# Kernel tuning notes

Hardware: AMD Instinct MI355X
Metric: run time of the kernel (lower is better)

Reference implementation:

```python
import jax, jax.numpy as jnp
import numpy as np

B, N, K, D = 2, 32768, 16, 64
EPS = 1e-6

def setup_inputs() -> dict:
    key = jax.random.key(0)
    k1, k2, k3, k4, k5, k6 = jax.random.split(key, 6)
    coords = jax.random.normal(k1, (B, N, 3), dtype=jnp.float32)
    features = jax.random.normal(k2, (B, D, N, 1), dtype=jnp.float32)
    idx = jax.random.randint(k3, (B, N, K), 0, N, dtype=jnp.int32)
    dist = jax.random.uniform(k4, (B, N, K), dtype=jnp.float32)
    conv_w = jax.random.normal(k5, (D, 10), dtype=jnp.float32) * 0.3  # 1x1 conv weight
    conv_b = jax.random.normal(k6, (D,), dtype=jnp.float32) * 0.01
    bn_gamma = jnp.ones((D,), dtype=jnp.float32)
    bn_beta = jnp.zeros((D,), dtype=jnp.float32)
    return {"coords": coords, "features": features, "dist": dist,
            "conv_w": conv_w, "conv_b": conv_b,
            "bn_gamma": bn_gamma, "bn_beta": bn_beta, "idx": idx}

def reference(coords, features, dist, conv_w, conv_b, bn_gamma, bn_beta, idx):
    # gather neighbor coords: (B, N, K, 3)
    neighbors = jax.vmap(lambda c, i: c[i])(coords, idx)
    center = jnp.broadcast_to(coords[:, :, None, :], (B, N, K, 3))
    # relative-position encoding: center | neighbor | center-neighbor | dist -> 10 channels
    concat = jnp.concatenate([center, neighbors, center - neighbors, dist[..., None]], axis=-1)
    # 1x1 conv == channel matmul: (B,N,K,10) @ (D,10)^T -> (B,N,K,D)
    x = jnp.einsum('bnkc,dc->bnkd', concat, conv_w) + conv_b
    # BatchNorm2d in training mode: batch stats over (B,N,K) per channel, eps=1e-6
    mean = jnp.mean(x, axis=(0, 1, 2))
    var = jnp.var(x, axis=(0, 1, 2))
    x = (x - mean) * jax.lax.rsqrt(var + EPS) * bn_gamma + bn_beta
    x = jax.nn.relu(x)
    x = jnp.transpose(x, (0, 3, 1, 2))  # (B, D, N, K)
    feat = jnp.broadcast_to(features, (B, D, N, K))
    return jnp.concatenate([x, feat], axis=1)  # (B, 2D, N, K)
```

## Files before the change

### kernel.cpp

```cpp
#include <hip/hip_runtime.h>

#define BB 2
#define NN 32768
#define KK 16
#define DD 64
#define NC 10
#define NMOM 65
#define NBLK1 256
#define BN_EPS 1e-6

__host__ __device__ __forceinline__ constexpr int pair_idx(int i, int j) {
    return 10 + i * 10 - (i * (i - 1)) / 2 + (j - i);
}

__global__ __launch_bounds__(256) void k_moments(
    const float* __restrict__ coords, const float* __restrict__ dist,
    const int* __restrict__ idx, float* __restrict__ partials)
{
    const int tid = threadIdx.x;
    const int bn = blockIdx.x * 256 + tid;
    const int b = bn >> 15;

    float acc[NMOM];
#pragma unroll
    for (int v = 0; v < NMOM; ++v) acc[v] = 0.f;

    const float cx = coords[(size_t)bn * 3 + 0];
    const float cy = coords[(size_t)bn * 3 + 1];
    const float cz = coords[(size_t)bn * 3 + 2];
    const float* cb = coords + (size_t)b * NN * 3;

    for (int k = 0; k < KK; ++k) {
        const int j = idx[(size_t)bn * KK + k];
        const float nx = cb[(size_t)j * 3 + 0];
        const float ny = cb[(size_t)j * 3 + 1];
        const float nz = cb[(size_t)j * 3 + 2];
        const float dd = dist[(size_t)bn * KK + k];
        const float c[NC] = {cx, cy, cz, nx, ny, nz, cx - nx, cy - ny, cz - nz, dd};
#pragma unroll
        for (int i = 0; i < NC; ++i) acc[i] += c[i];
#pragma unroll
        for (int i = 0; i < NC; ++i)
#pragma unroll
            for (int jj = i; jj < NC; ++jj)
                acc[pair_idx(i, jj)] += c[i] * c[jj];
    }

    __shared__ float red[4 * NMOM];
    const int lane = tid & 63, wave = tid >> 6;
#pragma unroll
    for (int v = 0; v < NMOM; ++v) {
        float x = acc[v];
        x += __shfl_down(x, 32);
        x += __shfl_down(x, 16);
        x += __shfl_down(x, 8);
        x += __shfl_down(x, 4);
        x += __shfl_down(x, 2);
        x += __shfl_down(x, 1);
        if (lane == 0) red[wave * NMOM + v] = x;
    }
    __syncthreads();
    if (tid < NMOM) {
        float p = red[tid] + red[NMOM + tid] + red[2 * NMOM + tid] + red[3 * NMOM + tid];
        partials[blockIdx.x * NMOM + tid] = p;
    }
}

__global__ __launch_bounds__(320) void k_finalize(
    const float* __restrict__ partials,
    const float* __restrict__ conv_w, const float* __restrict__ conv_b,
    const float* __restrict__ gamma, const float* __restrict__ beta,
    float* __restrict__ wscaled, float* __restrict__ bias2)
{
    __shared__ double part[4][NMOM];
    __shared__ double sums[NMOM];
    const int tid = threadIdx.x;
    const int g = tid / NMOM, m = tid % NMOM;
    if (g < 4) {
        double s = 0.0;
        for (int blk = g * 64; blk < (g + 1) * 64; ++blk)
            s += (double)partials[blk * NMOM + m];
        part[g][m] = s;
    }
    __syncthreads();
    if (tid < NMOM)
        sums[tid] = part[0][tid] + part[1][tid] + part[2][tid] + part[3][tid];
    __syncthreads();
    if (tid < DD) {
        const double cnt = (double)BB * NN * KK;
        double mm[NC], w[NC];
#pragma unroll
        for (int c = 0; c < NC; ++c) {
            mm[c] = sums[c] / cnt;
            w[c] = (double)conv_w[tid * NC + c];
        }
        const double bd = (double)conv_b[tid];
        double wm = 0.0;
#pragma unroll
        for (int c = 0; c < NC; ++c) wm += w[c] * mm[c];
        const double mean = wm + bd;
        double ex2 = bd * bd + 2.0 * bd * wm;
#pragma unroll
        for (int i = 0; i < NC; ++i)
#pragma unroll
            for (int j = i; j < NC; ++j) {
                const double Mij = sums[pair_idx(i, j)] / cnt;
                ex2 += (i == j ? 1.0 : 2.0) * w[i] * w[j] * Mij;
            }
        const double var = ex2 - mean * mean;
        const double scale = (double)gamma[tid] / sqrt(var + BN_EPS);
        bias2[tid] = (float)((double)beta[tid] + (bd - mean) * scale);
#pragma unroll
        for (int c = 0; c < NC; ++c)
            wscaled[tid * NC + c] = (float)(w[c] * scale);
    }
}

__global__ __launch_bounds__(256) void k_x(
    const float* __restrict__ coords, const float* __restrict__ dist,
    const int* __restrict__ idx,
    const float* __restrict__ wscaled, const float* __restrict__ bias2,
    float* __restrict__ out)
{
    __shared__ float c_lds[NC][1024];
    __shared__ float w_s[DD * NC];
    __shared__ float b2_s[DD];

    const int tid = threadIdx.x;
    for (int i = tid; i < DD * NC; i += 256) w_s[i] = wscaled[i];
    if (tid < DD) b2_s[tid] = bias2[tid];

    const int b  = blockIdx.x >> 9;
    const int n0 = (blockIdx.x & 511) << 6;

    {
        const int n_loc = tid >> 2;
        const int k0 = (tid & 3) << 2;
        const int bn = b * NN + n0 + n_loc;

        const float* cc = coords + (size_t)bn * 3;
        const float cx = cc[0], cy = cc[1], cz = cc[2];
        const float* cb = coords + (size_t)b * NN * 3;

        const int4 j4 = *reinterpret_cast<const int4*>(idx + (size_t)bn * KK + k0);
        const float4 d4 = *reinterpret_cast<const float4*>(dist + (size_t)bn * KK + k0);
        const int js[4] = {j4.x, j4.y, j4.z, j4.w};
        const float dsv[4] = {d4.x, d4.y, d4.z, d4.w};

        float c[4][NC];
#pragma unroll
        for (int q = 0; q < 4; ++q) {
            const float* nc = cb + (size_t)js[q] * 3;
            const float nx = nc[0], ny = nc[1], nz = nc[2];
            c[q][0] = cx; c[q][1] = cy; c[q][2] = cz;
            c[q][3] = nx; c[q][4] = ny; c[q][5] = nz;
            c[q][6] = cx - nx; c[q][7] = cy - ny; c[q][8] = cz - nz;
            c[q][9] = dsv[q];
        }
#pragma unroll
        for (int ch = 0; ch < NC; ++ch) {
            float4 v{c[0][ch], c[1][ch], c[2][ch], c[3][ch]};
            *reinterpret_cast<float4*>(&c_lds[ch][tid << 2]) = v;
        }
    }
    __syncthreads();

    const int lane = tid & 63, wave = tid >> 6;
    const size_t cstride = (size_t)NN * KK;
    const size_t base0 = (((size_t)b * 2 * DD) * NN + n0) * KK;

#pragma unroll 2
    for (int dd = 0; dd < 16; ++dd) {
        const int d = (wave << 4) + dd;
        float wv[NC];
#pragma unroll
        for (int ch = 0; ch < NC; ++ch) wv[ch] = w_s[d * NC + ch];
        const float b2 = b2_s[d];
        float* dst = out + base0 + (size_t)d * cstride;

#pragma unroll
        for (int chunk = 0; chunk < 4; ++chunk) {
            const int nk0 = (chunk << 8) + (lane << 2);
            float4 acc{b2, b2, b2, b2};
#pragma unroll
            for (int ch = 0; ch < NC; ++ch) {
                const float4 cv = *reinterpret_cast<const float4*>(&c_lds[ch][nk0]);
                const float w = wv[ch];
                acc.x += cv.x * w; acc.y += cv.y * w;
                acc.z += cv.z * w; acc.w += cv.w * w;
            }
            acc.x = fmaxf(acc.x, 0.f); acc.y = fmaxf(acc.y, 0.f);
            acc.z = fmaxf(acc.z, 0.f); acc.w = fmaxf(acc.w, 0.f);
            *reinterpret_cast<float4*>(dst + nk0) = acc;
        }
    }
}

__global__ __launch_bounds__(256) void k_feat(
    const float* __restrict__ features, float* __restrict__ out)
{
    const int t = blockIdx.x * 256 + threadIdx.x;
    const float f = features[t];
    const int bd = t >> 15;
    const int n = t & (NN - 1);
    const int b = bd >> 6;
    const int d = bd & (DD - 1);
    const size_t base = (((size_t)b * 2 * DD + DD + d) * NN + n) * KK;
    const float4 v{f, f, f, f};
    float4* p = reinterpret_cast<float4*>(out + base);
    p[0] = v; p[1] = v; p[2] = v; p[3] = v;
}

extern "C" void kernel_launch(void* const* d_in, const int* in_sizes, int n_in,
                              void* d_out, int out_size, void* d_ws, size_t ws_size,
                              hipStream_t stream) {
    const float* coords   = (const float*)d_in[0];
    const float* features = (const float*)d_in[1];
    const float* dist     = (const float*)d_in[2];
    const float* conv_w   = (const float*)d_in[3];
    const float* conv_b   = (const float*)d_in[4];
    const float* gamma    = (const float*)d_in[5];
    const float* beta     = (const float*)d_in[6];
    const int*   idx      = (const int*)d_in[7];
    float* out = (float*)d_out;

    float* partials = (float*)d_ws;
    float* wscaled  = partials + NBLK1 * NMOM;
    float* bias2    = wscaled + DD * NC;

    k_moments<<<NBLK1, 256, 0, stream>>>(coords, dist, idx, partials);
    k_finalize<<<1, 320, 0, stream>>>(partials, conv_w, conv_b, gamma, beta,
                                      wscaled, bias2);
    k_feat<<<(BB * DD * NN) / 256, 256, 0, stream>>>(features, out);
    k_x<<<BB * (NN / 64), 256, 0, stream>>>(
        coords, dist, idx, wscaled, bias2, out);
}
```

Measured before the change: 720.6 us.

## Materialize concat channels to workspace and fuse feature broadcast into output kernel

Splits the output stage into a kernel that writes the ten concat channels to a global channel-major buffer and a single output kernel that handles both the conv+BN+ReLU planes and the feature broadcast planes. Each output block writes one contiguous 16KB chunk of one channel plane instead of striding across 16 planes per block, and the separate feature kernel launch is removed. It adds about 42MB of extra buffer write plus reads per output channel, which will mostly hit cache, and it needs a larger workspace.

Result: faster. 642.6 us (-10.8%).

```diff
diff --git a/kernel.cpp b/kernel.cpp
--- a/kernel.cpp
+++ b/kernel.cpp
@@ -8,6 +8,7 @@
 #define NMOM 65
 #define NBLK1 256
 #define BN_EPS 1e-6
+#define BNK ((size_t)BB * NN * KK)
 
 __host__ __device__ __forceinline__ constexpr int pair_idx(int i, int j) {
     return 10 + i * 10 - (i * (i - 1)) / 2 + (j - i);
@@ -116,99 +117,91 @@
     }
 }
 
-__global__ __launch_bounds__(256) void k_x(
+__global__ __launch_bounds__(256) void k_c(
     const float* __restrict__ coords, const float* __restrict__ dist,
-    const int* __restrict__ idx,
+    const int* __restrict__ idx, float* __restrict__ cbuf)
+{
+    const int t = blockIdx.x * 256 + threadIdx.x;
+    const int e0 = t << 2;
+    const int bn = e0 >> 4;
+    const int k0 = e0 & 15;
+    const int b = bn >> 15;
+
+    const float* cc = coords + (size_t)bn * 3;
+    const float cx = cc[0], cy = cc[1], cz = cc[2];
+    const float* cb = coords + (size_t)b * NN * 3;
+
+    const int4 j4 = *reinterpret_cast<const int4*>(idx + (size_t)bn * KK + k0);
+    const float4 d4 = *reinterpret_cast<const float4*>(dist + (size_t)bn * KK + k0);
+    const int js[4] = {j4.x, j4.y, j4.z, j4.w};
+    const float dsv[4] = {d4.x, d4.y, d4.z, d4.w};
+
+    float c[4][NC];
+#pragma unroll
+    for (int q = 0; q < 4; ++q) {
+        const float* nc2 = cb + (size_t)js[q] * 3;
+        const float nx = nc2[0], ny = nc2[1], nz = nc2[2];
+        c[q][0] = cx; c[q][1] = cy; c[q][2] = cz;
+        c[q][3] = nx; c[q][4] = ny; c[q][5] = nz;
+        c[q][6] = cx - nx; c[q][7] = cy - ny; c[q][8] = cz - nz;
+        c[q][9] = dsv[q];
+    }
+#pragma unroll
+    for (int ch = 0; ch < NC; ++ch) {
+        float4 v{c[0][ch], c[1][ch], c[2][ch], c[3][ch]};
+        *reinterpret_cast<float4*>(&cbuf[(size_t)ch * BNK + e0]) = v;
+    }
+}
+
+__global__ __launch_bounds__(256) void k_out(
+    const float* __restrict__ cbuf, const float* __restrict__ features,
     const float* __restrict__ wscaled, const float* __restrict__ bias2,
     float* __restrict__ out)
 {
-    __shared__ float c_lds[NC][1024];
-    __shared__ float w_s[DD * NC];
-    __shared__ float b2_s[DD];
-
+    const int nc  = blockIdx.x & 127;
+    const int ch2 = (blockIdx.x >> 7) & 127;
+    const int b   = blockIdx.x >> 14;
     const int tid = threadIdx.x;
-    for (int i = tid; i < DD * NC; i += 256) w_s[i] = wscaled[i];
-    if (tid < DD) b2_s[tid] = bias2[tid];
-
-    const int b  = blockIdx.x >> 9;
-    const int n0 = (blockIdx.x & 511) << 6;
-
-    {
-        const int n_loc = tid >> 2;
-        const int k0 = (tid & 3) << 2;
-        const int bn = b * NN + n0 + n_loc;
-
-        const float* cc = coords + (size_t)bn * 3;
-        const float cx = cc[0], cy = cc[1], cz = cc[2];
-        const float* cb = coords + (size_t)b * NN * 3;
-
-        const int4 j4 = *reinterpret_cast<const int4*>(idx + (size_t)bn * KK + k0);
-        const float4 d4 = *reinterpret_cast<const float4*>(dist + (size_t)bn * KK + k0);
-        const int js[4] = {j4.x, j4.y, j4.z, j4.w};
-        const float dsv[4] = {d4.x, d4.y, d4.z, d4.w};
-
-        float c[4][NC];
-#pragma unroll
-        for (int q = 0; q < 4; ++q) {
-            const float* nc = cb + (size_t)js[q] * 3;
-            const float nx = nc[0], ny = nc[1], nz = nc[2];
-            c[q][0] = cx; c[q][1] = cy; c[q][2] = cz;
-            c[q][3] = nx; c[q][4] = ny; c[q][5] = nz;
-            c[q][6] = cx - nx; c[q][7] = cy - ny; c[q][8] = cz - nz;
-            c[q][9] = dsv[q];
+    const size_t plane = ((size_t)b * 2 * DD + ch2) * ((size_t)NN * KK);
+
+    if (ch2 < DD) {
+        const int d = ch2;
+        float wv[NC];
+#pragma unroll
+        for (int ch = 0; ch < NC; ++ch) wv[ch] = wscaled[d * NC + ch];
+        const float b2 = bias2[d];
+        const size_t locbase = (size_t)nc * 256 * KK;
+        const size_t ebase = (size_t)b * NN * KK + locbase;
+
+#pragma unroll
+        for (int j = 0; j < 4; ++j) {
+            const size_t off = (size_t)(j * 1024 + tid * 4);
+            float4 a{b2, b2, b2, b2};
+#pragma unroll
+            for (int ch = 0; ch < NC; ++ch) {
+                const float4 cv = *reinterpret_cast<const float4*>(
+                    &cbuf[(size_t)ch * BNK + ebase + off]);
+                const float w = wv[ch];
+                a.x += cv.x * w; a.y += cv.y * w;
+                a.z += cv.z * w; a.w += cv.w * w;
+            }
+            a.x = fmaxf(a.x, 0.f); a.y = fmaxf(a.y, 0.f);
+            a.z = fmaxf(a.z, 0.f); a.w = fmaxf(a.w, 0.f);
+            *reinterpret_cast<float4*>(out + plane + locbase + off) = a;
         }
-#pragma unroll
-        for (int ch = 0; ch < NC; ++ch) {
-            float4 v{c[0][ch], c[1][ch], c[2][ch], c[3][ch]};
-            *reinterpret_cast<float4*>(&c_lds[ch][tid << 2]) = v;
+    } else {
+        const int d = ch2 - DD;
+        const float* fb = features + ((size_t)b * DD + d) * NN;
+        const size_t locbase = (size_t)nc * 256 * KK;
+#pragma unroll
+        for (int j = 0; j < 4; ++j) {
+            const int q = j * 256 + tid;
+            const int n = nc * 256 + (q >> 2);
+            const float f = fb[n];
+            *reinterpret_cast<float4*>(out + plane + locbase + (size_t)q * 4) =
+                float4{f, f, f, f};
         }
     }
-    __syncthreads();
-
-    const int lane = tid & 63, wave = tid >> 6;
-    const size_t cstride = (size_t)NN * KK;
-    const size_t base0 = (((size_t)b * 2 * DD) * NN + n0) * KK;
-
-#pragma unroll 2
-    for (int dd = 0; dd < 16; ++dd) {
-        const int d = (wave << 4) + dd;
-        float wv[NC];
-#pragma unroll
-        for (int ch = 0; ch < NC; ++ch) wv[ch] = w_s[d * NC + ch];
-        const float b2 = b2_s[d];
-        float* dst = out + base0 + (size_t)d * cstride;
-
-#pragma unroll
-        for (int chunk = 0; chunk < 4; ++chunk) {
-            const int nk0 = (chunk << 8) + (lane << 2);
-            float4 acc{b2, b2, b2, b2};
-#pragma unroll
-            for (int ch = 0; ch < NC; ++ch) {
-                const float4 cv = *reinterpret_cast<const float4*>(&c_lds[ch][nk0]);
-                const float w = wv[ch];
-                acc.x += cv.x * w; acc.y += cv.y * w;
-                acc.z += cv.z * w; acc.w += cv.w * w;
-            }
-            acc.x = fmaxf(acc.x, 0.f); acc.y = fmaxf(acc.y, 0.f);
-            acc.z = fmaxf(acc.z, 0.f); acc.w = fmaxf(acc.w, 0.f);
-            *reinterpret_cast<float4*>(dst + nk0) = acc;
-        }
-    }
-}
-
-__global__ __launch_bounds__(256) void k_feat(
-    const float* __restrict__ features, float* __restrict__ out)
-{
-    const int t = blockIdx.x * 256 + threadIdx.x;
-    const float f = features[t];
-    const int bd = t >> 15;
-    const int n = t & (NN - 1);
-    const int b = bd >> 6;
-    const int d = bd & (DD - 1);
-    const size_t base = (((size_t)b * 2 * DD + DD + d) * NN + n) * KK;
-    const float4 v{f, f, f, f};
-    float4* p = reinterpret_cast<float4*>(out + base);
-    p[0] = v; p[1] = v; p[2] = v; p[3] = v;
 }
 
 extern "C" void kernel_launch(void* const* d_in, const int* in_sizes, int n_in,
@@ -227,11 +220,11 @@
     float* partials = (float*)d_ws;
     float* wscaled  = partials + NBLK1 * NMOM;
     float* bias2    = wscaled + DD * NC;
+    float* cbuf     = (float*)d_ws + 65536;
 
     k_moments<<<NBLK1, 256, 0, stream>>>(coords, dist, idx, partials);
     k_finalize<<<1, 320, 0, stream>>>(partials, conv_w, conv_b, gamma, beta,
                                       wscaled, bias2);
-    k_feat<<<(BB * DD * NN) / 256, 256, 0, stream>>>(features, out);
-    k_x<<<BB * (NN / 64), 256, 0, stream>>>(
-        coords, dist, idx, wscaled, bias2, out);
-}
+    k_c<<<(int)(BNK / 4 / 256), 256, 0, stream>>>(coords, dist, idx, cbuf);
+    k_out<<<BB * 128 * 128, 256, 0, stream>>>(cbuf, features, wscaled, bias2, out);
+}
```
